# Performance work log

Hardware: AMD Instinct MI355X
Metric: run time of the kernel (lower is better)

The kernel has to match this reference:

```python
import jax, jax.numpy as jnp
import numpy as np

DIM_IN = 1024
DIM_OUT = 1024
B = 8192


def setup_inputs() -> dict:
    key = jax.random.key(0)
    ks = jax.random.split(key, 8)
    d = DIM_IN + DIM_OUT
    bound = 1.0 / np.sqrt(d)
    def lin(kw, kb):
        W = jax.random.uniform(kw, (d, DIM_OUT), jnp.float32, -bound, bound)
        b = jax.random.uniform(kb, (DIM_OUT,), jnp.float32, -bound, bound)
        return W, b
    kx, kh, kc, kp = ks[0], ks[1], ks[2], ks[3]
    pw = jax.random.split(kp, 8)
    W_I, b_I = lin(pw[0], pw[1])
    W_F, b_F = lin(pw[2], pw[3])
    W_G, b_G = lin(pw[4], pw[5])
    W_O, b_O = lin(pw[6], pw[7])
    return {
        "x": jax.random.normal(kx, (B, DIM_IN), jnp.float32),
        "h": jax.random.normal(kh, (B, DIM_OUT), jnp.float32),
        "c": jax.random.normal(kc, (B, DIM_OUT), jnp.float32),
        "W_I": W_I, "b_I": b_I,
        "W_F": W_F, "b_F": b_F,
        "W_G": W_G, "b_G": b_G,
        "W_O": W_O, "b_O": b_O,
    }


def reference(x, h, c, W_I, b_I, W_F, b_F, W_G, b_G, W_O, b_O):
    X = jnp.concatenate([x, h], axis=-1)  # [B, dimIn+dimOut]
    # Fuse the 4 gate projections into one GEMM: [B,d] @ [d, 4*dimOut]
    W = jnp.concatenate([W_I, W_F, W_G, W_O], axis=1)
    b = jnp.concatenate([b_I, b_F, b_G, b_O], axis=0)
    gates = X @ W + b
    i_, f_, g_, o_ = jnp.split(gates, 4, axis=-1)
    I = jax.nn.sigmoid(i_)
    F = jax.nn.sigmoid(f_)
    G = jnp.tanh(g_)
    O = jax.nn.sigmoid(o_)
    C = F * c + I * G
    return O * jnp.tanh(C), C
```

## Files before the change

### kernel.cpp

```cpp
#include <hip/hip_runtime.h>
#include <cstdint>


#define B_ROWS 8192
#define DK 2048
#define DOUT 1024
#define TM 128
#define TN 128
#define BK 32

typedef __bf16 bf16x8 __attribute__((ext_vector_type(8)));
typedef __bf16 bf16x4 __attribute__((ext_vector_type(4)));
typedef float f32x4 __attribute__((ext_vector_type(4)));

__device__ inline void load16_to_lds(const __bf16* gsrc, __bf16* ldst) {
    __builtin_amdgcn_global_load_lds(
        (const __attribute__((address_space(1))) void*)gsrc,
        (__attribute__((address_space(3))) void*)ldst,
        16, 0, 0);
}

__device__ inline float fast_sigmoid(float x) {
    return __builtin_amdgcn_rcpf(1.0f + __builtin_amdgcn_exp2f(-1.442695041f * x));
}
__device__ inline float fast_tanh(float x) {
    return 1.0f - 2.0f * __builtin_amdgcn_rcpf(1.0f + __builtin_amdgcn_exp2f(2.885390082f * x));
}

__global__ __launch_bounds__(256) void prep_x(const float* __restrict__ x,
                                              const float* __restrict__ h,
                                              __bf16* __restrict__ X) {
    int id = blockIdx.x * 256 + threadIdx.x;
    int b = id >> 9;
    int k = (id & 511) * 4;
    float4 v;
    if (k < 1024) v = *(const float4*)&x[(size_t)b * 1024 + k];
    else          v = *(const float4*)&h[(size_t)b * 1024 + (k - 1024)];
    bf16x4 o = { (__bf16)v.x, (__bf16)v.y, (__bf16)v.z, (__bf16)v.w };
    *(bf16x4*)&X[(size_t)b * 2048 + k] = o;
}

__global__ __launch_bounds__(256) void prep_w(const float* __restrict__ WI,
                                              const float* __restrict__ WF,
                                              const float* __restrict__ WG,
                                              const float* __restrict__ WO,
                                              __bf16* __restrict__ Wt) {
    int kb = blockIdx.x;
    int jb = blockIdx.y;
    int j0 = jb * 32;
    __shared__ float t[32][33];
    int tx = threadIdx.x, ty = threadIdx.y;
    const float* Ws[4] = {WI, WF, WG, WO};
#pragma unroll
    for (int g = 0; g < 4; ++g) {
        const float* W = Ws[g];
#pragma unroll
        for (int yy = 0; yy < 32; yy += 8) {
            int k = kb * 32 + ty + yy;
            t[ty + yy][tx] = W[(size_t)k * 1024 + j0 + tx];
        }
        __syncthreads();
#pragma unroll
        for (int yy = 0; yy < 32; yy += 8) {
            int r = ty + yy;
            int npp = (jb * 2 + (r >> 4)) * 64 + g * 16 + (r & 15);
            Wt[(size_t)npp * 2048 + kb * 32 + tx] = (__bf16)t[tx][r];
        }
        __syncthreads();
    }
}

__global__ __launch_bounds__(256) void lstm_gemm(
    const __bf16* __restrict__ Xbf, const __bf16* __restrict__ Wt,
    const float* __restrict__ c,
    const float* __restrict__ bI, const float* __restrict__ bF,
    const float* __restrict__ bG, const float* __restrict__ bO,
    float* __restrict__ outH, float* __restrict__ outC)
{
    __shared__ __bf16 As[TM * BK];
    __shared__ __bf16 Bs[TN * BK];

    const int t = threadIdx.x;
    const int lane = t & 63;
    const int wave = t >> 6;
    const int wm = wave >> 1;
    const int wn = wave & 1;
    const int m0 = blockIdx.x * TM;
    const int nb = blockIdx.y;
    const int n0 = nb * TN;

    f32x4 acc[4][4];
#pragma unroll
    for (int i = 0; i < 4; ++i)
#pragma unroll
        for (int j = 0; j < 4; ++j) acc[i][j] = (f32x4){0.f, 0.f, 0.f, 0.f};

    const int r0 = t >> 2, kc0 = (t & 3) * 8;
    const int r1 = 64 + r0;
    const __bf16* gA0 = Xbf + (size_t)(m0 + r0) * DK + kc0;
    const __bf16* gA1 = Xbf + (size_t)(m0 + r1) * DK + kc0;
    const __bf16* gB0 = Wt + (size_t)(n0 + r0) * DK + kc0;
    const __bf16* gB1 = Wt + (size_t)(n0 + r1) * DK + kc0;
    __bf16* lA0 = As + wave * 512;
    __bf16* lA1 = As + 2048 + wave * 512;
    __bf16* lB0 = Bs + wave * 512;
    __bf16* lB1 = Bs + 2048 + wave * 512;

    const int lr = lane & 15;
    const int kh = (lane >> 4) * 8;
    const int arow = wm * 64 + lr;
    const int brow = wn * 64 + lr;

    for (int kk = 0; kk < DK / BK; ++kk) {
        load16_to_lds(gA0, lA0);
        load16_to_lds(gA1, lA1);
        load16_to_lds(gB0, lB0);
        load16_to_lds(gB1, lB1);
        gA0 += BK; gA1 += BK; gB0 += BK; gB1 += BK;
        __syncthreads();

        bf16x8 a[4], b[4];
#pragma unroll
        for (int i = 0; i < 4; ++i)
            a[i] = *(const bf16x8*)&As[(arow + i * 16) * BK + kh];
#pragma unroll
        for (int j = 0; j < 4; ++j)
            b[j] = *(const bf16x8*)&Bs[(brow + j * 16) * BK + kh];
#pragma unroll
        for (int i = 0; i < 4; ++i)
#pragma unroll
            for (int j = 0; j < 4; ++j)
                acc[i][j] = __builtin_amdgcn_mfma_f32_16x16x32_bf16(a[i], b[j], acc[i][j], 0, 0, 0);
        __syncthreads();
    }

    const int col = lane & 15;
    const int j = (nb * 2 + wn) * 16 + col;
    const float biI = bI[j], biF = bF[j], biG = bG[j], biO = bO[j];
    const int rbase = m0 + wm * 64 + (lane >> 4) * 4;
#pragma unroll
    for (int i = 0; i < 4; ++i) {
#pragma unroll
        for (int r = 0; r < 4; ++r) {
            int row = rbase + i * 16 + r;
            float I = fast_sigmoid(acc[i][0][r] + biI);
            float F = fast_sigmoid(acc[i][1][r] + biF);
            float G = fast_tanh(acc[i][2][r] + biG);
            float O = fast_sigmoid(acc[i][3][r] + biO);
            size_t idx = (size_t)row * DOUT + j;
            float Cn = F * c[idx] + I * G;
            outH[idx] = O * fast_tanh(Cn);
            outC[idx] = Cn;
        }
    }
}

extern "C" void kernel_launch(void* const* d_in, const int* in_sizes, int n_in,
                              void* d_out, int out_size, void* d_ws, size_t ws_size,
                              hipStream_t stream) {
    const float* x  = (const float*)d_in[0];
    const float* h  = (const float*)d_in[1];
    const float* c  = (const float*)d_in[2];
    const float* WI = (const float*)d_in[3];
    const float* bI = (const float*)d_in[4];
    const float* WF = (const float*)d_in[5];
    const float* bF = (const float*)d_in[6];
    const float* WG = (const float*)d_in[7];
    const float* bG = (const float*)d_in[8];
    const float* WO = (const float*)d_in[9];
    const float* bO = (const float*)d_in[10];

    __bf16* Xbf = (__bf16*)d_ws;
    __bf16* Wt  = (__bf16*)((char*)d_ws + (size_t)B_ROWS * DK * 2);
    float* outH = (float*)d_out;
    float* outC = outH + (size_t)B_ROWS * DOUT;

    prep_x<<<(B_ROWS * DK / 4) / 256, 256, 0, stream>>>(x, h, Xbf);
    prep_w<<<dim3(DK / 32, DOUT / 32), dim3(32, 8), 0, stream>>>(WI, WF, WG, WO, Wt);
    lstm_gemm<<<dim3(B_ROWS / TM, 4 * DOUT / TN), 256, 0, stream>>>(
        Xbf, Wt, c, bI, bF, bG, bO, outH, outC);
}
```

Before: 357.7 us.

## Double GEMM K-tile to 64 and widen prep kernels' vector stores

```diff
diff --git a/kernel.cpp b/kernel.cpp
--- a/kernel.cpp
+++ b/kernel.cpp
@@ -7,7 +7,7 @@
 #define DOUT 1024
 #define TM 128
 #define TN 128
-#define BK 32
+#define BK 64
 
 typedef __bf16 bf16x8 __attribute__((ext_vector_type(8)));
 typedef __bf16 bf16x4 __attribute__((ext_vector_type(4)));
@@ -31,13 +31,15 @@
                                               const float* __restrict__ h,
                                               __bf16* __restrict__ X) {
     int id = blockIdx.x * 256 + threadIdx.x;
-    int b = id >> 9;
-    int k = (id & 511) * 4;
-    float4 v;
-    if (k < 1024) v = *(const float4*)&x[(size_t)b * 1024 + k];
-    else          v = *(const float4*)&h[(size_t)b * 1024 + (k - 1024)];
-    bf16x4 o = { (__bf16)v.x, (__bf16)v.y, (__bf16)v.z, (__bf16)v.w };
-    *(bf16x4*)&X[(size_t)b * 2048 + k] = o;
+    int b = id >> 8;
+    int k = (id & 255) * 8;
+    const float* src = (k < 1024) ? &x[(size_t)b * 1024 + k]
+                                  : &h[(size_t)b * 1024 + (k - 1024)];
+    float4 v0 = *(const float4*)src;
+    float4 v1 = *(const float4*)(src + 4);
+    bf16x8 o = { (__bf16)v0.x, (__bf16)v0.y, (__bf16)v0.z, (__bf16)v0.w,
+                 (__bf16)v1.x, (__bf16)v1.y, (__bf16)v1.z, (__bf16)v1.w };
+    *(bf16x8*)&X[(size_t)b * 2048 + k] = o;
 }
 
 __global__ __launch_bounds__(256) void prep_w(const float* __restrict__ WI,
@@ -48,23 +50,28 @@
     int kb = blockIdx.x;
     int jb = blockIdx.y;
     int j0 = jb * 32;
-    __shared__ float t[32][33];
+    __shared__ float t[64][33];
     int tx = threadIdx.x, ty = threadIdx.y;
+    int idx = ty * 32 + tx;
     const float* Ws[4] = {WI, WF, WG, WO};
 #pragma unroll
     for (int g = 0; g < 4; ++g) {
         const float* W = Ws[g];
 #pragma unroll
-        for (int yy = 0; yy < 32; yy += 8) {
-            int k = kb * 32 + ty + yy;
+        for (int yy = 0; yy < 64; yy += 8) {
+            int k = kb * 64 + ty + yy;
             t[ty + yy][tx] = W[(size_t)k * 1024 + j0 + tx];
         }
         __syncthreads();
 #pragma unroll
-        for (int yy = 0; yy < 32; yy += 8) {
-            int r = ty + yy;
+        for (int w = 0; w < 2; ++w) {
+            int slot = w * 256 + idx;
+            int r = slot >> 4;
+            int k0 = (slot & 15) * 4;
+            bf16x4 o = { (__bf16)t[k0 + 0][r], (__bf16)t[k0 + 1][r],
+                         (__bf16)t[k0 + 2][r], (__bf16)t[k0 + 3][r] };
             int npp = (jb * 2 + (r >> 4)) * 64 + g * 16 + (r & 15);
-            Wt[(size_t)npp * 2048 + kb * 32 + tx] = (__bf16)t[tx][r];
+            *(bf16x4*)&Wt[(size_t)npp * 2048 + kb * 64 + k0] = o;
         }
         __syncthreads();
     }
@@ -95,16 +102,12 @@
 #pragma unroll
         for (int j = 0; j < 4; ++j) acc[i][j] = (f32x4){0.f, 0.f, 0.f, 0.f};
 
-    const int r0 = t >> 2, kc0 = (t & 3) * 8;
-    const int r1 = 64 + r0;
-    const __bf16* gA0 = Xbf + (size_t)(m0 + r0) * DK + kc0;
-    const __bf16* gA1 = Xbf + (size_t)(m0 + r1) * DK + kc0;
-    const __bf16* gB0 = Wt + (size_t)(n0 + r0) * DK + kc0;
-    const __bf16* gB1 = Wt + (size_t)(n0 + r1) * DK + kc0;
-    __bf16* lA0 = As + wave * 512;
-    __bf16* lA1 = As + 2048 + wave * 512;
-    __bf16* lB0 = Bs + wave * 512;
-    __bf16* lB1 = Bs + 2048 + wave * 512;
+    const int rs = t >> 3;
+    const int kc = (t & 7) * 8;
+    const __bf16* gA = Xbf + (size_t)(m0 + rs) * DK + kc;
+    const __bf16* gB = Wt + (size_t)(n0 + rs) * DK + kc;
+    __bf16* lA = As + wave * 512;
+    __bf16* lB = Bs + wave * 512;
 
     const int lr = lane & 15;
     const int kh = (lane >> 4) * 8;
@@ -112,25 +115,29 @@
     const int brow = wn * 64 + lr;
 
     for (int kk = 0; kk < DK / BK; ++kk) {
-        load16_to_lds(gA0, lA0);
-        load16_to_lds(gA1, lA1);
-        load16_to_lds(gB0, lB0);
-        load16_to_lds(gB1, lB1);
-        gA0 += BK; gA1 += BK; gB0 += BK; gB1 += BK;
+#pragma unroll
+        for (int q = 0; q < 4; ++q) {
+            load16_to_lds(gA + (size_t)(q * 32) * DK, lA + q * 2048);
+            load16_to_lds(gB + (size_t)(q * 32) * DK, lB + q * 2048);
+        }
+        gA += BK; gB += BK;
         __syncthreads();
 
-        bf16x8 a[4], b[4];
 #pragma unroll
-        for (int i = 0; i < 4; ++i)
-            a[i] = *(const bf16x8*)&As[(arow + i * 16) * BK + kh];
+        for (int ks = 0; ks < BK; ks += 32) {
+            bf16x8 a[4], b[4];
 #pragma unroll
-        for (int j = 0; j < 4; ++j)
-            b[j] = *(const bf16x8*)&Bs[(brow + j * 16) * BK + kh];
-#pragma unroll
-        for (int i = 0; i < 4; ++i)
+            for (int i = 0; i < 4; ++i)
+                a[i] = *(const bf16x8*)&As[(arow + i * 16) * BK + ks + kh];
 #pragma unroll
             for (int j = 0; j < 4; ++j)
-                acc[i][j] = __builtin_amdgcn_mfma_f32_16x16x32_bf16(a[i], b[j], acc[i][j], 0, 0, 0);
+                b[j] = *(const bf16x8*)&Bs[(brow + j * 16) * BK + ks + kh];
+#pragma unroll
+            for (int i = 0; i < 4; ++i)
+#pragma unroll
+                for (int j = 0; j < 4; ++j)
+                    acc[i][j] = __builtin_amdgcn_mfma_f32_16x16x32_bf16(a[i], b[j], acc[i][j], 0, 0, 0);
+        }
         __syncthreads();
     }
 
@@ -175,8 +182,8 @@
     float* outH = (float*)d_out;
     float* outC = outH + (size_t)B_ROWS * DOUT;
 
-    prep_x<<<(B_ROWS * DK / 4) / 256, 256, 0, stream>>>(x, h, Xbf);
-    prep_w<<<dim3(DK / 32, DOUT / 32), dim3(32, 8), 0, stream>>>(WI, WF, WG, WO, Wt);
+    prep_x<<<(B_ROWS * DK / 8) / 256, 256, 0, stream>>>(x, h, Xbf);
+    prep_w<<<dim3(DK / 64, DOUT / 32), dim3(32, 8), 0, stream>>>(WI, WF, WG, WO, Wt);
     lstm_gemm<<<dim3(B_ROWS / TM, 4 * DOUT / TN), 256, 0, stream>>>(
         Xbf, Wt, c, bI, bF, bG, bO, outH, outC);
 }
```

New measurement: 367.8 us. 1.03x slower.
